# Performance work log

Hardware: AMD Instinct MI355X
Metric: run time of the kernel (lower is better)

The kernel has to match this reference:

```python
import jax, jax.numpy as jnp
from jax import lax
import numpy as np

TAU = 10.0      # tauSr == tauRef
THR = 1.0       # theta
WIDTH = 1.0     # tauRho (surrogate width)
SCALE = 1.0     # scaleRho (surrogate scale)
DECAY = float(np.exp(-1.0 / TAU))


@jax.custom_vjp
def _heaviside(v):
    # spike = 1[v >= theta]
    return (v >= THR).astype(v.dtype)

def _heaviside_fwd(v):
    return _heaviside(v), v

def _heaviside_bwd(v, g):
    # SLAYER exponential surrogate pdf: scaleRho/tauRho * exp(-|v-theta|/tauRho)
    return (g * (SCALE / WIDTH) * jnp.exp(-jnp.abs(v - THR) / WIDTH),)

_heaviside.defvjp(_heaviside_fwd, _heaviside_bwd)


def _conv2d(x, w, pad):
    # x: (B, Cin, H, W), w: (Cout, Cin, kh, kw); SLAYER convs have no bias
    return lax.conv_general_dilated(
        x, w, window_strides=(1, 1), padding=[(pad, pad), (pad, pad)],
        dimension_numbers=("NCHW", "OIHW", "NCHW"))


def _sumpool(x, k):
    # SLAYER pool = sum over kxk window (times a learned scalar applied outside)
    B, C, H, W = x.shape
    return x.reshape(B, C, H // k, k, W // k, k).sum(axis=(3, 5))


def _psp(seq):
    # exponential synaptic (PSP) filter along time: s[t] = a*s[t-1] + x[t]
    a = jnp.asarray(DECAY, seq.dtype)
    def step(s, x_t):
        s = a * s + x_t
        return s, s
    _, out = lax.scan(step, jnp.zeros_like(seq[0]), seq)
    return out  # (T, ...)


def _spikes(u):
    # thresholded spiking with decaying refractory feedback (scaleRef=1):
    # v[t] = u[t] - r[t]; s[t] = 1[v >= theta]; r[t+1] = b*(r[t] + theta*s[t])
    b = jnp.asarray(DECAY, u.dtype)
    def step(r, u_t):
        s = _heaviside(u_t - r)
        r_next = b * (r + THR * s)
        return r_next, s
    _, out = lax.scan(step, jnp.zeros_like(u[0]), u)
    return out  # (T, ...)


def _forward(x, conv1_w, conv2_w, lin_w, w_pool1, w_pool2):
    N, T, C, H, W = x.shape  # (64, 100, 2, 32, 32)
    h = _conv2d(x.reshape(N * T, C, H, W), conv1_w, 2)        # (NT, 4, 32, 32)
    h = _sumpool(h, 4) * w_pool1                               # (NT, 4, 8, 8)
    h = h.reshape(N, T, 4, 8, 8).swapaxes(0, 1)                # (T, N, 4, 8, 8)
    s1 = _spikes(_psp(h))                                      # (T, N, 4, 8, 8)
    h2 = _conv2d(s1.reshape(T * N, 4, 8, 8), conv2_w, 1)       # (TN, 8, 8, 8)
    h2 = (_sumpool(h2, 2) * w_pool2).reshape(T, N, 8, 4, 4)    # (T, N, 8, 4, 4)
    s2 = _spikes(_psp(h2))                                     # (T, N, 8, 4, 4)
    # dense = full-spatial conv (2, 8, 4, 4) -> (N, T, 2)
    return jnp.einsum("tnchw,ochw->nto", s2, lin_w)


def setup_inputs() -> dict:
    key = jax.random.key(0)
    ks = jax.random.split(key, 4)
    x = (jax.random.uniform(ks[0], (64, 100, 2, 32, 32)) < 0.1).astype(jnp.float32)
    conv1_w = jax.random.normal(ks[1], (4, 2, 5, 5), jnp.float32) * 0.3
    conv2_w = jax.random.normal(ks[2], (8, 4, 3, 3), jnp.float32) * 0.3
    lin_w = jax.random.normal(ks[3], (2, 8, 4, 4), jnp.float32) * 0.3
    w_pool1 = jnp.float32(1.0 / 16.0)  # 1.1*theta / (16 * 1.1)
    w_pool2 = jnp.float32(1.0 / 4.0)   # 1.1*theta / (4 * 1.1)
    return {"x": x, "conv1_w": conv1_w, "conv2_w": conv2_w, "lin_w": lin_w,
            "w_pool1": w_pool1, "w_pool2": w_pool2}


def reference(x, conv1_w, conv2_w, lin_w, w_pool1, w_pool2):
    return _forward(x, conv1_w, conv2_w, lin_w, w_pool1, w_pool2)
```

## Files before the change

kernel.cpp:

```cpp
#include <hip/hip_runtime.h>


#define DECAY 0.9048374180359595f

#define BAR_LGKM() asm volatile("s_waitcnt lgkmcnt(0)\n\ts_barrier" ::: "memory")
#define FENCE_LGKM() asm volatile("s_waitcnt lgkmcnt(0)" ::: "memory")

__global__ __launch_bounds__(128) void k0_fold(const float* __restrict__ w1,
        const float* __restrict__ w2, const float* __restrict__ wp1,
        const float* __restrict__ wp2, float* __restrict__ wl1,
        float* __restrict__ wl2, float* __restrict__ out) {
    const int tid = threadIdx.x;
    out[blockIdx.x * 128 + tid] = 0.f;
    if (blockIdx.x != 0) return;
    const float p1 = wp1[0], p2 = wp2[0];
    for (int idx = tid; idx < 512; idx += 128) {
        const int f = idx & 7, c = (idx >> 3) & 3, e = (idx >> 5) & 7, cin = idx >> 8;
        const int cc = c * 2 + cin;
        int alo = e - 3; if (alo < 0) alo = 0;
        int ahi = e;     if (ahi > 4) ahi = 4;
        int blo = f - 3; if (blo < 0) blo = 0;
        int bhi = f;     if (bhi > 4) bhi = 4;
        float s = 0.f;
        for (int a = alo; a <= ahi; ++a)
            for (int b = blo; b <= bhi; ++b)
                s += w1[cc * 25 + a * 5 + b];
        wl1[(cin * 8 + e) * 32 + c * 8 + f] = s * p1;
    }
    for (int idx = tid; idx < 512; idx += 128) {
        const int c2 = idx & 7, f = (idx >> 3) & 3, e = (idx >> 5) & 3, cin = idx >> 7;
        int alo = e - 1; if (alo < 0) alo = 0;
        int ahi = e;     if (ahi > 2) ahi = 2;
        int blo = f - 1; if (blo < 0) blo = 0;
        int bhi = f;     if (bhi > 2) bhi = 2;
        float s = 0.f;
        for (int aa = alo; aa <= ahi; ++aa)
            for (int bb = blo; bb <= bhi; ++bb)
                s += w2[((c2 * 4 + cin) * 3 + aa) * 3 + bb];
        wl2[c2 * 68 + cin * 16 + e * 4 + f] = s * p2;
    }
}

__global__ __launch_bounds__(64) void k1(const float* __restrict__ x,
        const float* __restrict__ wg, float* __restrict__ u1) {
    __shared__ __align__(16) float xs[2 * 1296];
    __shared__ __align__(16) float wl[512];
    const int lane = threadIdx.x;
    const int frame = blockIdx.x;
    const int n = frame / 100, t = frame % 100;

    *(float4*)(wl + 4 * lane)       = *(const float4*)(wg + 4 * lane);
    *(float4*)(wl + 256 + 4 * lane) = *(const float4*)(wg + 256 + 4 * lane);

    #pragma unroll
    for (int m0 = 0; m0 < 128; m0 += 64) {
        const int m = m0 + lane;
        if (m < 72) {
            const int cin = m / 36, rem = m % 36;
            const int rr = rem / 9, q4 = rem % 9;
            const int pr = (rr == 0) ? 0 : (rr == 1) ? 9 : (rr == 2) ? 26 : 35;
            *(float4*)(xs + cin * 1296 + pr * 36 + q4 * 4) = make_float4(0.f, 0.f, 0.f, 0.f);
        }
    }
    #pragma unroll
    for (int m0 = 0; m0 < 192; m0 += 64) {
        const int m = m0 + lane;
        if (m < 144) {
            const int cin = m / 72, rem = m % 72;
            const int side = rem & 1, pr = rem >> 1;
            *(float2*)(xs + cin * 1296 + pr * 36 + side * 34) = make_float2(0.f, 0.f);
        }
    }
    const float4* xg = (const float4*)(x + (size_t)frame * 2048);
    #pragma unroll
    for (int q = 0; q < 8; ++q) {
        const int m = q * 64 + lane;
        const float4 v = xg[m];
        const int li = 4 * m;
        const int cin = li >> 10, row = (li >> 5) & 31, col = li & 31;
        const int r = row + 2;
        const int pr = (r & 3) * 9 + (r >> 2);
        float* d = xs + cin * 1296 + pr * 36 + col + 2;
        *(float2*)(d)     = make_float2(v.x, v.y);
        *(float2*)(d + 2) = make_float2(v.z, v.w);
    }
    FENCE_LGKM();

    const int cp = lane >> 5;
    const int i  = (lane >> 2) & 7;
    const int jh = (lane >> 1) & 1;
    const int eh = lane & 1;

    float acc[2][4] = {{0.f, 0.f, 0.f, 0.f}, {0.f, 0.f, 0.f, 0.f}};
    const float* tb = xs + (i + eh) * 36 + jh * 16;
    #pragma unroll
    for (int cin = 0; cin < 2; ++cin) {
        #pragma unroll
        for (int et = 0; et < 4; ++et) {
            const int ro = cin * 1296 + et * 9 * 36;
            float xr[20];
            #pragma unroll
            for (int b = 0; b < 5; ++b)
                *(float4*)(xr + 4 * b) = *(const float4*)(tb + ro + 4 * b);
            float wv[16];
            const float* wp = wl + (cin * 8 + eh * 4 + et) * 32 + cp * 16;
            #pragma unroll
            for (int q = 0; q < 4; ++q)
                *(float4*)(wv + 4 * q) = *(const float4*)(wp + 4 * q);
            #pragma unroll
            for (int cl = 0; cl < 2; ++cl) {
                #pragma unroll
                for (int jj = 0; jj < 4; ++jj) {
                    const int o = 4 * jj;
                    acc[cl][jj] += xr[o]*wv[cl*8]     + xr[o+1]*wv[cl*8+1]
                                 + xr[o+2]*wv[cl*8+2] + xr[o+3]*wv[cl*8+3]
                                 + xr[o+4]*wv[cl*8+4] + xr[o+5]*wv[cl*8+5]
                                 + xr[o+6]*wv[cl*8+6] + xr[o+7]*wv[cl*8+7];
                }
            }
        }
    }
    #pragma unroll
    for (int cl = 0; cl < 2; ++cl)
        #pragma unroll
        for (int jj = 0; jj < 4; ++jj)
            acc[cl][jj] += __shfl_xor(acc[cl][jj], 1);

    const float o0 = eh ? acc[1][0] : acc[0][0];
    const float o1 = eh ? acc[1][1] : acc[0][1];
    const float o2 = eh ? acc[1][2] : acc[0][2];
    const float o3 = eh ? acc[1][3] : acc[0][3];
    *(float4*)(u1 + (size_t)t * 16384 + n * 256 + (2 * cp + eh) * 64 + i * 8 + jh * 4) =
        make_float4(o0, o1, o2, o3);
}

__global__ __launch_bounds__(256) void kf(const float* __restrict__ u1,
        const float* __restrict__ wl2g, const float* __restrict__ lw,
        float* __restrict__ out) {
    __shared__ __align__(16) float ls1[100 * 260];
    __shared__ __align__(16) float ls2[100 * 36];
    const int tid = threadIdx.x;
    const int bid = blockIdx.x;
    const int n = (bid & 7) * 8 + (bid >> 5);
    const int qtr = (bid >> 3) & 3;
    const int wave = tid >> 6, l64 = tid & 63;
    const float a = DECAY;

    const float* up = u1 + n * 256 + tid;

    const int sub = tid >> 4, l16 = tid & 15;
    const int c2l = l16 >> 3, i2 = (l16 >> 1) & 3, jhp = l16 & 1;
    const int c2g = qtr * 2 + c2l;

    float4 wreg[16];
    {
        const float* wbase = wl2g + c2g * 68;
        #pragma unroll
        for (int q = 0; q < 16; ++q)
            wreg[q] = *(const float4*)(wbase + (q >> 2) * 16 + (q & 3) * 4);
    }

    const int cell = l64 & 31;
    const float w0 = lw[qtr * 32 + cell];
    const float w1 = lw[128 + qtr * 32 + cell];

    float vbuf[100];
    #pragma unroll
    for (int k = 0; k < 100; ++k) vbuf[k] = up[(size_t)k * 16384];
    {
        float psp = 0.f, rr = 0.f;
        #pragma unroll
        for (int k = 0; k < 100; ++k) {
            psp = a * psp + vbuf[k];
            const float vv = psp - rr;
            const float s = (vv >= 1.f) ? 1.f : 0.f;
            rr = a * (rr + s);
            ls1[k * 260 + tid] = s;
        }
    }
    BAR_LGKM();

    #pragma unroll 1
    for (int pass = 0; pass < 7; ++pass) {
        const int slot = sub + 16 * pass;
        if (slot < 100) {
            const float* sb = ls1 + slot * 260;
            float acc0 = 0.f, acc1 = 0.f;
            #pragma unroll
            for (int cin = 0; cin < 4; ++cin) {
                #pragma unroll
                for (int e = 0; e < 4; ++e) {
                    const int ri = 2 * i2 + e - 1;
                    const int rc = (ri < 0) ? 0 : (ri > 7 ? 7 : ri);
                    const bool rok = (ri >= 0) && (ri <= 7);
                    float rr8[8];
                    const float* rp = sb + cin * 64 + rc * 8;
                    *(float4*)(rr8)     = *(const float4*)(rp);
                    *(float4*)(rr8 + 4) = *(const float4*)(rp + 4);
                    float xr[6];
                    xr[0] = jhp ? rr8[3] : 0.0f;
                    xr[1] = jhp ? rr8[4] : rr8[0];
                    xr[2] = jhp ? rr8[5] : rr8[1];
                    xr[3] = jhp ? rr8[6] : rr8[2];
                    xr[4] = jhp ? rr8[7] : rr8[3];
                    xr[5] = jhp ? 0.0f   : rr8[4];
                    if (!rok) {
                        #pragma unroll
                        for (int m = 0; m < 6; ++m) xr[m] = 0.0f;
                    }
                    const float4 wf = wreg[cin * 4 + e];
                    acc0 += xr[0] * wf.x; acc0 += xr[1] * wf.y;
                    acc0 += xr[2] * wf.z; acc0 += xr[3] * wf.w;
                    acc1 += xr[2] * wf.x; acc1 += xr[3] * wf.y;
                    acc1 += xr[4] * wf.z; acc1 += xr[5] * wf.w;
                }
            }
            *(float2*)(ls2 + slot * 36 + c2l * 16 + i2 * 4 + 2 * jhp) =
                make_float2(acc0, acc1);
        }
    }
    BAR_LGKM();

    if (wave == 0 && l64 < 32) {
        float ub[100];
        #pragma unroll
        for (int k = 0; k < 100; ++k) ub[k] = ls2[k * 36 + l64];
        float psp2 = 0.f, rr2 = 0.f;
        #pragma unroll
        for (int k = 0; k < 100; ++k) {
            psp2 = a * psp2 + ub[k];
            const float vv = psp2 - rr2;
            const float s = (vv >= 1.f) ? 1.f : 0.f;
            rr2 = a * (rr2 + s);
            const unsigned long long b = __ballot(s != 0.f);
            if (b) {
                float p0 = s * w0, p1 = s * w1;
                #pragma unroll
                for (int m = 16; m >= 1; m >>= 1) {
                    p0 += __shfl_xor(p0, m);
                    p1 += __shfl_xor(p1, m);
                }
                if (l64 == 0) {
                    atomicAdd(&out[n * 200 + k * 2],     p0);
                    atomicAdd(&out[n * 200 + k * 2 + 1], p1);
                }
            }
        }
    }
}

extern "C" void kernel_launch(void* const* d_in, const int* in_sizes, int n_in,
                              void* d_out, int out_size, void* d_ws, size_t ws_size,
                              hipStream_t stream) {
    const float* x   = (const float*)d_in[0];
    const float* w1  = (const float*)d_in[1];
    const float* w2  = (const float*)d_in[2];
    const float* lw  = (const float*)d_in[3];
    const float* wp1 = (const float*)d_in[4];
    const float* wp2 = (const float*)d_in[5];

    float* u1  = (float*)d_ws;
    float* wl1 = u1 + 1638400;
    float* wl2 = wl1 + 512;
    float* out = (float*)d_out;

    k0_fold<<<100, 128, 0, stream>>>(w1, w2, wp1, wp2, wl1, wl2, out);
    k1<<<6400, 64, 0, stream>>>(x, wl1, u1);
    kf<<<256, 256, 0, stream>>>(u1, wl2, lw, out);
}
```

Baseline: 125.8 us.

## Split kf across output channels with fp16 spike LDS and parallel dense reduction

```diff
diff --git a/kernel.cpp b/kernel.cpp
--- a/kernel.cpp
+++ b/kernel.cpp
@@ -5,6 +5,8 @@
 
 #define BAR_LGKM() asm volatile("s_waitcnt lgkmcnt(0)\n\ts_barrier" ::: "memory")
 #define FENCE_LGKM() asm volatile("s_waitcnt lgkmcnt(0)" ::: "memory")
+
+typedef __attribute__((ext_vector_type(8))) _Float16 half8;
 
 __global__ __launch_bounds__(128) void k0_fold(const float* __restrict__ w1,
         const float* __restrict__ w2, const float* __restrict__ wp1,
@@ -134,35 +136,30 @@
         make_float4(o0, o1, o2, o3);
 }
 
-__global__ __launch_bounds__(256) void kf(const float* __restrict__ u1,
+__global__ __launch_bounds__(256, 2) void kf(const float* __restrict__ u1,
         const float* __restrict__ wl2g, const float* __restrict__ lw,
         float* __restrict__ out) {
-    __shared__ __align__(16) float ls1[100 * 260];
-    __shared__ __align__(16) float ls2[100 * 36];
+    __shared__ __align__(16) _Float16 ls1h[100 * 264];
+    __shared__ __align__(16) float    ls2[100 * 20];
     const int tid = threadIdx.x;
     const int bid = blockIdx.x;
-    const int n = (bid & 7) * 8 + (bid >> 5);
-    const int qtr = (bid >> 3) & 3;
+    const int n   = (bid & 7) * 8 + (bid >> 6);
+    const int oct = (bid >> 3) & 7;
     const int wave = tid >> 6, l64 = tid & 63;
     const float a = DECAY;
 
     const float* up = u1 + n * 256 + tid;
 
-    const int sub = tid >> 4, l16 = tid & 15;
-    const int c2l = l16 >> 3, i2 = (l16 >> 1) & 3, jhp = l16 & 1;
-    const int c2g = qtr * 2 + c2l;
+    const int sub = tid >> 3, l8 = tid & 7;
+    const int i2 = l8 >> 1, jhp = l8 & 1;
 
     float4 wreg[16];
     {
-        const float* wbase = wl2g + c2g * 68;
+        const float* wbase = wl2g + oct * 68;
         #pragma unroll
         for (int q = 0; q < 16; ++q)
             wreg[q] = *(const float4*)(wbase + (q >> 2) * 16 + (q & 3) * 4);
     }
-
-    const int cell = l64 & 31;
-    const float w0 = lw[qtr * 32 + cell];
-    const float w1 = lw[128 + qtr * 32 + cell];
 
     float vbuf[100];
     #pragma unroll
@@ -175,16 +172,16 @@
             const float vv = psp - rr;
             const float s = (vv >= 1.f) ? 1.f : 0.f;
             rr = a * (rr + s);
-            ls1[k * 260 + tid] = s;
+            ls1h[k * 264 + tid] = (_Float16)s;
         }
     }
     BAR_LGKM();
 
     #pragma unroll 1
-    for (int pass = 0; pass < 7; ++pass) {
-        const int slot = sub + 16 * pass;
+    for (int pass = 0; pass < 4; ++pass) {
+        const int slot = sub + 32 * pass;
         if (slot < 100) {
-            const float* sb = ls1 + slot * 260;
+            const _Float16* sb = ls1h + slot * 264;
             float acc0 = 0.f, acc1 = 0.f;
             #pragma unroll
             for (int cin = 0; cin < 4; ++cin) {
@@ -193,10 +190,10 @@
                     const int ri = 2 * i2 + e - 1;
                     const int rc = (ri < 0) ? 0 : (ri > 7 ? 7 : ri);
                     const bool rok = (ri >= 0) && (ri <= 7);
+                    const half8 hv = *(const half8*)(sb + cin * 64 + rc * 8);
                     float rr8[8];
-                    const float* rp = sb + cin * 64 + rc * 8;
-                    *(float4*)(rr8)     = *(const float4*)(rp);
-                    *(float4*)(rr8 + 4) = *(const float4*)(rp + 4);
+                    #pragma unroll
+                    for (int m = 0; m < 8; ++m) rr8[m] = (float)hv[m];
                     float xr[6];
                     xr[0] = jhp ? rr8[3] : 0.0f;
                     xr[1] = jhp ? rr8[4] : rr8[0];
@@ -215,16 +212,16 @@
                     acc1 += xr[4] * wf.z; acc1 += xr[5] * wf.w;
                 }
             }
-            *(float2*)(ls2 + slot * 36 + c2l * 16 + i2 * 4 + 2 * jhp) =
+            *(float2*)(ls2 + slot * 20 + i2 * 4 + 2 * jhp) =
                 make_float2(acc0, acc1);
         }
     }
     BAR_LGKM();
 
-    if (wave == 0 && l64 < 32) {
+    if (wave == 0 && l64 < 16) {
         float ub[100];
         #pragma unroll
-        for (int k = 0; k < 100; ++k) ub[k] = ls2[k * 36 + l64];
+        for (int k = 0; k < 100; ++k) ub[k] = ls2[k * 20 + l64];
         float psp2 = 0.f, rr2 = 0.f;
         #pragma unroll
         for (int k = 0; k < 100; ++k) {
@@ -232,20 +229,29 @@
             const float vv = psp2 - rr2;
             const float s = (vv >= 1.f) ? 1.f : 0.f;
             rr2 = a * (rr2 + s);
-            const unsigned long long b = __ballot(s != 0.f);
-            if (b) {
-                float p0 = s * w0, p1 = s * w1;
-                #pragma unroll
-                for (int m = 16; m >= 1; m >>= 1) {
-                    p0 += __shfl_xor(p0, m);
-                    p1 += __shfl_xor(p1, m);
-                }
-                if (l64 == 0) {
-                    atomicAdd(&out[n * 200 + k * 2],     p0);
-                    atomicAdd(&out[n * 200 + k * 2 + 1], p1);
-                }
-            }
-        }
+            ls2[k * 20 + l64] = s;
+        }
+    }
+    BAR_LGKM();
+
+    if (tid < 200) {
+        const int t = tid >> 1, o = tid & 1;
+        const float* srow = ls2 + t * 20;
+        const float* wrow = lw + o * 128 + oct * 16;
+        const float4 s0 = *(const float4*)(srow);
+        const float4 s1 = *(const float4*)(srow + 4);
+        const float4 s2 = *(const float4*)(srow + 8);
+        const float4 s3 = *(const float4*)(srow + 12);
+        const float4 w0 = *(const float4*)(wrow);
+        const float4 w1 = *(const float4*)(wrow + 4);
+        const float4 w2 = *(const float4*)(wrow + 8);
+        const float4 w3 = *(const float4*)(wrow + 12);
+        float v = 0.f;
+        v += s0.x * w0.x; v += s0.y * w0.y; v += s0.z * w0.z; v += s0.w * w0.w;
+        v += s1.x * w1.x; v += s1.y * w1.y; v += s1.z * w1.z; v += s1.w * w1.w;
+        v += s2.x * w2.x; v += s2.y * w2.y; v += s2.z * w2.z; v += s2.w * w2.w;
+        v += s3.x * w3.x; v += s3.y * w3.y; v += s3.z * w3.z; v += s3.w * w3.w;
+        atomicAdd(&out[n * 200 + t * 2 + o], v);
     }
 }
 
@@ -266,5 +272,5 @@
 
     k0_fold<<<100, 128, 0, stream>>>(w1, w2, wp1, wp2, wl1, wl2, out);
     k1<<<6400, 64, 0, stream>>>(x, wl1, u1);
-    kf<<<256, 256, 0, stream>>>(u1, wl2, lw, out);
-}
+    kf<<<512, 256, 0, stream>>>(u1, wl2, lw, out);
+}
```

New measurement: 117.6 us (median of 4 runs). -6.5%, faster.
